# Kernel optimization log

Measured on AMD Instinct MI355X. Metric: run time of the kernel, lower is better.

Reference implementation:

```python
import jax, jax.numpy as jnp
import numpy as np

H, D_IN, D_Q, D_V = 8, 16, 32, 32
N = M = 4096


def setup_inputs() -> dict:
    key = jax.random.key(0)
    ks = jax.random.split(key, 12)
    s_in = 1.0 / np.sqrt(D_IN)
    s_fc = 1.0 / np.sqrt(H * D_V)
    return {
        "x": jax.random.normal(ks[0], (N, D_IN), jnp.float32),
        "y": jax.random.normal(ks[1], (M, D_IN), jnp.float32),
        # per-head stacked weights: [H, D_IN, D_Q/ D_V]
        "Wq": jax.random.uniform(ks[2], (H, D_IN, D_Q), jnp.float32, -s_in, s_in),
        "bq": jax.random.uniform(ks[3], (H, D_Q), jnp.float32, -s_in, s_in),
        "Wk": jax.random.uniform(ks[4], (H, D_IN, D_Q), jnp.float32, -s_in, s_in),
        "bk": jax.random.uniform(ks[5], (H, D_Q), jnp.float32, -s_in, s_in),
        "Wv": jax.random.uniform(ks[6], (H, D_IN, D_V), jnp.float32, -s_in, s_in),
        "bv": jax.random.uniform(ks[7], (H, D_V), jnp.float32, -s_in, s_in),
        "Wo": jax.random.uniform(ks[8], (H * D_V, D_IN), jnp.float32, -s_fc, s_fc),
        "bo": jax.random.uniform(ks[9], (D_IN,), jnp.float32, -s_fc, s_fc),
    }


def reference(x, y, Wq, bq, Wk, bk, Wv, bv, Wo, bo):
    # batched per-head projections (fuses the 8 tiny Linears of the torch loop)
    q = jnp.einsum("nd,hdq->hnq", x, Wq) + bq[:, None, :]   # [H, N, D_Q]
    k = jnp.einsum("md,hdq->hmq", y, Wk) + bk[:, None, :]   # [H, M, D_Q]
    v = jnp.einsum("md,hdv->hmv", y, Wv) + bv[:, None, :]   # [H, M, D_V]
    scores = jnp.einsum("hnq,hmq->hnm", q, k) / jnp.sqrt(jnp.float32(D_Q))
    attn = jax.nn.softmax(scores, axis=-1)                  # [H, N, M]
    heads = jnp.einsum("hnm,hmv->hnv", attn, v)             # [H, N, D_V]
    # torch.cat(head_outputs, dim=-1): head h occupies columns [h*D_V:(h+1)*D_V]
    concat = jnp.transpose(heads, (1, 0, 2)).reshape(x.shape[0], H * D_V)
    return concat @ Wo + bo                                  # [N, D_IN]
```

## Files before the change

kernel.cpp:

```cpp
#include <hip/hip_runtime.h>
#include <hip/hip_bf16.h>

typedef __attribute__((ext_vector_type(8))) short bf16x8;
typedef __attribute__((ext_vector_type(4))) float f32x4;
typedef unsigned short u16;
typedef unsigned int u32;

#define NH 8
#define NN 4096
#define MM 4096

__device__ __forceinline__ u16 f2bf(float f) {
  u32 b = __float_as_uint(f);
  b += 0x7FFFu + ((b >> 16) & 1u);
  return (u16)(b >> 16);
}

__device__ __forceinline__ u32 pack_rnu(float a, float b) {
  u32 ua = __float_as_uint(a) + 0x8000u;
  u32 ub = __float_as_uint(b) + 0x8000u;
#if __has_builtin(__builtin_amdgcn_perm)
  return __builtin_amdgcn_perm(ub, ua, 0x07060302u);
#else
  return (ua >> 16) | (ub & 0xFFFF0000u);
#endif
}

#if __has_builtin(__builtin_amdgcn_exp2f)
__device__ __forceinline__ float exp2_fast(float x) { return __builtin_amdgcn_exp2f(x); }
#else
__device__ __forceinline__ float exp2_fast(float x) { return __expf(x * 0.69314718055994531f); }
#endif

__global__ __launch_bounds__(256) void proj_kernel(
    const float* __restrict__ x, const float* __restrict__ y,
    const float* __restrict__ Wq, const float* __restrict__ bq,
    const float* __restrict__ Wk, const float* __restrict__ bk,
    const float* __restrict__ Wv, const float* __restrict__ bv,
    u16* __restrict__ qs, u16* __restrict__ ks, u16* __restrict__ vT)
{
  __shared__ u16 sv[256][33];
  const int bid = blockIdx.x;
  const int tid = threadIdx.x;
  if (bid < 256) {
    int idx = bid * 256 + tid;
    int t = idx >> 15;
    int h = (idx >> 12) & 7;
    int row = idx & 4095;
    const float* src = (t ? y : x) + row * 16;
    const float* W = (t ? Wk : Wq) + (h << 9);
    const float* b = (t ? bk : bq) + (h << 5);
    const float scale = t ? 1.0f : 0.25503635116465163f;
    float4 r4[4];
#pragma unroll
    for (int i = 0; i < 4; ++i) r4[i] = ((const float4*)src)[i];
    const float* r = (const float*)r4;
    u16* out = (t ? ks : qs) + (idx & 32767) * 32;
#pragma unroll
    for (int j = 0; j < 32; ++j) {
      float a = b[j];
#pragma unroll
      for (int i = 0; i < 16; ++i) a = fmaf(r[i], W[i * 32 + j], a);
      out[j] = f2bf(a * scale);
    }
  } else {
    int vb = bid - 256;
    int h = vb >> 4;
    int kb = (vb & 15) << 8;
    const float* src = y + (kb + tid) * 16;
    const float* W = Wv + (h << 9);
    const float* b = bv + (h << 5);
    float4 r4[4];
#pragma unroll
    for (int i = 0; i < 4; ++i) r4[i] = ((const float4*)src)[i];
    const float* r = (const float*)r4;
#pragma unroll
    for (int j = 0; j < 32; ++j) {
      float a = b[j];
#pragma unroll
      for (int i = 0; i < 16; ++i) a = fmaf(r[i], W[i * 32 + j], a);
      sv[tid][j] = f2bf(a);
    }
    __syncthreads();
    int dv = tid >> 3;
    int c = (tid & 7) << 5;
    u16* dst = vT + (((h << 5) + dv) << 12) + kb + c;
#pragma unroll
    for (int q = 0; q < 4; ++q) {
      uint4 w;
      w.x = (u32)sv[c + 4 * q + 0][dv]      | ((u32)sv[c + 4 * q + 1][dv] << 16);
      w.y = (u32)sv[c + 4 * q + 2][dv]      | ((u32)sv[c + 4 * q + 3][dv] << 16);
      w.z = (u32)sv[c + 16 + 4 * q + 0][dv] | ((u32)sv[c + 16 + 4 * q + 1][dv] << 16);
      w.w = (u32)sv[c + 16 + 4 * q + 2][dv] | ((u32)sv[c + 16 + 4 * q + 3][dv] << 16);
      *(uint4*)(dst + q * 8) = w;
    }
  }
}

#define KST 40
#define VST 72
#define VSZ (32 * VST)

__global__ __launch_bounds__(256) void flash_kernel(
    const u16* __restrict__ qs, const u16* __restrict__ ksrc,
    const u16* __restrict__ vT, float* __restrict__ accP,
    float* __restrict__ lsumP)
{
  __shared__ u16 sK[128 * KST];
  __shared__ u16 sVT[2 * VSZ];
  const int h = blockIdx.y;
  const int qt = blockIdx.x;
  const int z = blockIdx.z;
  const int nIter = (MM / 128) / gridDim.z;
  const int kb0 = z * (MM / gridDim.z);
  const int tid = threadIdx.x;
  const int wv = tid >> 6;
  const int lane = tid & 63;
  const int d = lane & 15;
  const int g = lane >> 4;
  const int qrowA = (qt << 7) + (wv << 5) + d;
  const int qrowB = qrowA + 16;

  union U4 { uint4 q; bf16x8 v; };
  U4 qfA, qfB;
  qfA.q = *(const uint4*)(qs + (((h << 12) + qrowA) << 5) + (g << 3));
  qfB.q = *(const uint4*)(qs + (((h << 12) + qrowB) << 5) + (g << 3));

  float lsA = 0.f, lsB = 0.f;
  f32x4 accA0 = {0.f, 0.f, 0.f, 0.f}, accA1 = {0.f, 0.f, 0.f, 0.f};
  f32x4 accB0 = {0.f, 0.f, 0.f, 0.f}, accB1 = {0.f, 0.f, 0.f, 0.f};
  const f32x4 zero = {0.f, 0.f, 0.f, 0.f};

  const u16* gK = ksrc + (h << 17) + (kb0 << 5) + ((tid >> 1) << 5) + ((tid & 1) << 4);
  const u16* gV = vT + (((h << 5) + (tid >> 3)) << 12) + kb0 + ((tid & 7) << 4);
  u16* wK = sK + (tid >> 1) * KST + ((tid & 1) << 4);
  u16* wV = sVT + ((tid & 7) >> 2) * VSZ + (tid >> 3) * VST + ((tid & 7) & 3) * 16;

  {
    uint4 a = *(const uint4*)gK, b = *(const uint4*)(gK + 8);
    uint4 c = *(const uint4*)gV, e = *(const uint4*)(gV + 8);
    *(uint4*)wK = a; *(uint4*)(wK + 8) = b;
    *(uint4*)wV = c; *(uint4*)(wV + 8) = e;
  }
  __syncthreads();

  auto compute = [&](const u16* kb, const u16* vb) {
    U4 kf0, kf1, kf2, kf3;
    kf0.q = *(const uint4*)(kb + (0 * 16 + d) * KST + (g << 3));
    kf1.q = *(const uint4*)(kb + (1 * 16 + d) * KST + (g << 3));
    kf2.q = *(const uint4*)(kb + (2 * 16 + d) * KST + (g << 3));
    kf3.q = *(const uint4*)(kb + (3 * 16 + d) * KST + (g << 3));
    U4 vf0, vf1, vf2, vf3;
    {
      const u16* vp = vb + d * VST;
      vf0.q = *(const uint4*)(vp + (g << 3));
      vf1.q = *(const uint4*)(vp + 32 + (g << 3));
      vp += 16 * VST;
      vf2.q = *(const uint4*)(vp + (g << 3));
      vf3.q = *(const uint4*)(vp + 32 + (g << 3));
    }
#define QTILE(QF, ACC0, ACC1, LS)                                              \
    {                                                                          \
      f32x4 s0, s1, s2, s3;                                                    \
      s0 = __builtin_amdgcn_mfma_f32_16x16x32_bf16(kf0.v, QF.v, zero, 0, 0, 0);\
      s1 = __builtin_amdgcn_mfma_f32_16x16x32_bf16(kf1.v, QF.v, zero, 0, 0, 0);\
      s2 = __builtin_amdgcn_mfma_f32_16x16x32_bf16(kf2.v, QF.v, zero, 0, 0, 0);\
      s3 = __builtin_amdgcn_mfma_f32_16x16x32_bf16(kf3.v, QF.v, zero, 0, 0, 0);\
      float e0 = exp2_fast(s0.x), e1 = exp2_fast(s0.y);                        \
      float e2 = exp2_fast(s0.z), e3 = exp2_fast(s0.w);                        \
      float e4 = exp2_fast(s1.x), e5 = exp2_fast(s1.y);                        \
      float e6 = exp2_fast(s1.z), e7 = exp2_fast(s1.w);                        \
      float e8 = exp2_fast(s2.x), e9 = exp2_fast(s2.y);                        \
      float e10 = exp2_fast(s2.z), e11 = exp2_fast(s2.w);                      \
      float e12 = exp2_fast(s3.x), e13 = exp2_fast(s3.y);                      \
      float e14 = exp2_fast(s3.z), e15 = exp2_fast(s3.w);                      \
      LS += (((e0 + e1) + (e2 + e3)) + ((e4 + e5) + (e6 + e7)))                \
          + (((e8 + e9) + (e10 + e11)) + ((e12 + e13) + (e14 + e15)));         \
      union { u32 w[4]; bf16x8 v; } pb0, pb1;                                  \
      pb0.w[0] = pack_rnu(e0, e1);   pb0.w[1] = pack_rnu(e2, e3);              \
      pb0.w[2] = pack_rnu(e4, e5);   pb0.w[3] = pack_rnu(e6, e7);              \
      pb1.w[0] = pack_rnu(e8, e9);   pb1.w[1] = pack_rnu(e10, e11);            \
      pb1.w[2] = pack_rnu(e12, e13); pb1.w[3] = pack_rnu(e14, e15);            \
      ACC0 = __builtin_amdgcn_mfma_f32_16x16x32_bf16(vf0.v, pb0.v, ACC0, 0, 0, 0); \
      ACC0 = __builtin_amdgcn_mfma_f32_16x16x32_bf16(vf1.v, pb1.v, ACC0, 0, 0, 0); \
      ACC1 = __builtin_amdgcn_mfma_f32_16x16x32_bf16(vf2.v, pb0.v, ACC1, 0, 0, 0); \
      ACC1 = __builtin_amdgcn_mfma_f32_16x16x32_bf16(vf3.v, pb1.v, ACC1, 0, 0, 0); \
    }
    QTILE(qfA, accA0, accA1, lsA)
    QTILE(qfB, accB0, accB1, lsB)
#undef QTILE
  };

#pragma unroll 1
  for (int it = 0; it < nIter; ++it) {
    uint4 a, b, c, e;
    if (it < nIter - 1) {
      gK += 4096; gV += 128;
      a = *(const uint4*)gK; b = *(const uint4*)(gK + 8);
      c = *(const uint4*)gV; e = *(const uint4*)(gV + 8);
    }
    compute(sK, sVT);
    compute(sK + 64 * KST, sVT + VSZ);
    __syncthreads();
    if (it < nIter - 1) {
      *(uint4*)wK = a; *(uint4*)(wK + 8) = b;
      *(uint4*)wV = c; *(uint4*)(wV + 8) = e;
      __syncthreads();
    }
  }

  lsA += __shfl_xor(lsA, 16);  lsA += __shfl_xor(lsA, 32);
  lsB += __shfl_xor(lsB, 16);  lsB += __shfl_xor(lsB, 32);
  if (g == 0) {
    lsumP[((z * NH + h) << 12) + qrowA] = lsA;
    lsumP[((z * NH + h) << 12) + qrowB] = lsB;
  }
  float* cpA = accP + z * (NN * 256) + (qrowA << 8) + (h << 5) + (g << 2);
  *(float4*)cpA        = make_float4(accA0.x, accA0.y, accA0.z, accA0.w);
  *(float4*)(cpA + 16) = make_float4(accA1.x, accA1.y, accA1.z, accA1.w);
  float* cpB = accP + z * (NN * 256) + (qrowB << 8) + (h << 5) + (g << 2);
  *(float4*)cpB        = make_float4(accB0.x, accB0.y, accB0.z, accB0.w);
  *(float4*)(cpB + 16) = make_float4(accB1.x, accB1.y, accB1.z, accB1.w);
}

__global__ __launch_bounds__(256) void out_fused_kernel(
    const float* __restrict__ accP, const float* __restrict__ lsumP,
    const float* __restrict__ Wo, const float* __restrict__ bo,
    float* __restrict__ out, int S)
{
  __shared__ float cn[4][256];
  __shared__ float sQ[4][4][16];
  const int tid = threadIdx.x;
  const int n0 = blockIdx.x << 2;

  {
    const int r = tid >> 6, u = tid & 63;
    const int n = n0 + r;
    float4 o = make_float4(0.f, 0.f, 0.f, 0.f);
    for (int s = 0; s < S; ++s) {
      const float4 v = *(const float4*)(accP + (size_t)s * (NN * 256) + (n << 8) + (u << 2));
      o.x += v.x; o.y += v.y; o.z += v.z; o.w += v.w;
    }
    const int hh = u >> 3;
    float l = 0.f;
    for (int s = 0; s < S; ++s) l += lsumP[((s * NH + hh) << 12) + n];
    const float inv = 1.0f / l;
    *(float4*)&cn[r][u << 2] = make_float4(o.x * inv, o.y * inv, o.z * inv, o.w * inv);
  }
  __syncthreads();

  {
    const int r = tid >> 6, ks = (tid >> 4) & 3, c = tid & 15;
    const float* cr = &cn[r][ks << 6];
    const float* wp = Wo + (ks << 6) * 16 + c;
    float a = 0.f;
#pragma unroll
    for (int jj = 0; jj < 64; ++jj) {
      const int j2 = (jj + (ks << 4)) & 63;
      a = fmaf(cr[j2], wp[j2 * 16], a);
    }
    sQ[r][ks][c] = a;
  }
  __syncthreads();

  if (tid < 64) {
    const int r = tid >> 4, c = tid & 15;
    float v = bo[c] + ((sQ[r][0][c] + sQ[r][1][c]) + (sQ[r][2][c] + sQ[r][3][c]));
    out[((n0 + r) << 4) + c] = v;
  }
}

extern "C" void kernel_launch(void* const* d_in, const int* in_sizes, int n_in,
                              void* d_out, int out_size, void* d_ws, size_t ws_size,
                              hipStream_t stream) {
  const float* x  = (const float*)d_in[0];
  const float* y  = (const float*)d_in[1];
  const float* Wq = (const float*)d_in[2];
  const float* bq = (const float*)d_in[3];
  const float* Wk = (const float*)d_in[4];
  const float* bk = (const float*)d_in[5];
  const float* Wv = (const float*)d_in[6];
  const float* bv = (const float*)d_in[7];
  const float* Wo = (const float*)d_in[8];
  const float* bo = (const float*)d_in[9];
  float* out = (float*)d_out;

  u16* qs = (u16*)d_ws;
  u16* ks = qs + (NH * NN * 32);
  u16* vT = ks + (NH * MM * 32);
  float* accP = (float*)(vT + (NH * MM * 32));
  int S = 1;
  if (ws_size >= (size_t)(6 + 32 + 2) * 1024 * 1024) S = 8;
  else if (ws_size >= (size_t)(6 + 16 + 1) * 1024 * 1024) S = 4;
  float* lsumP = accP + (size_t)S * (NN * 256);

  hipLaunchKernelGGL(proj_kernel, dim3(384), dim3(256), 0, stream,
                     x, y, Wq, bq, Wk, bk, Wv, bv, qs, ks, vT);
  hipLaunchKernelGGL(flash_kernel, dim3(32, NH, S), dim3(256), 0, stream,
                     qs, ks, vT, accP, lsumP);
  hipLaunchKernelGGL(out_fused_kernel, dim3(1024), dim3(256), 0, stream,
                     accP, lsumP, Wo, bo, out, S);
}
```

Measured before the change: 66.79 us.

## Load flash K/V fragments straight from global and split output stage

The flash kernel stops staging K and V tiles through shared memory. Each wave now loads its MFMA fragments directly from global memory and prefetches the next 64-key step into registers, which removes the LDS writes and both per-iteration __syncthreads. The grid is flattened with the head index varying fastest, and the key split is fixed at 4. The fused output kernel is replaced by an in-place combine kernel plus a separate output GEMM that keeps Wo in LDS. The cost is that the four waves of a block each read the same K/V from global or L2, one more kernel launch is added, and S=4 no longer adapts to the workspace size.

```diff
diff --git a/kernel.cpp b/kernel.cpp
--- a/kernel.cpp
+++ b/kernel.cpp
@@ -97,22 +97,16 @@
   }
 }
 
-#define KST 40
-#define VST 72
-#define VSZ (32 * VST)
-
 __global__ __launch_bounds__(256) void flash_kernel(
     const u16* __restrict__ qs, const u16* __restrict__ ksrc,
     const u16* __restrict__ vT, float* __restrict__ accP,
     float* __restrict__ lsumP)
 {
-  __shared__ u16 sK[128 * KST];
-  __shared__ u16 sVT[2 * VSZ];
-  const int h = blockIdx.y;
-  const int qt = blockIdx.x;
-  const int z = blockIdx.z;
-  const int nIter = (MM / 128) / gridDim.z;
-  const int kb0 = z * (MM / gridDim.z);
+  const int bid = blockIdx.x;
+  const int h = bid & 7;
+  const int qt = (bid >> 3) & 31;
+  const int z = bid >> 8;
+  const int kb0 = z << 10;
   const int tid = threadIdx.x;
   const int wv = tid >> 6;
   const int lane = tid & 63;
@@ -131,33 +125,32 @@
   f32x4 accB0 = {0.f, 0.f, 0.f, 0.f}, accB1 = {0.f, 0.f, 0.f, 0.f};
   const f32x4 zero = {0.f, 0.f, 0.f, 0.f};
 
-  const u16* gK = ksrc + (h << 17) + (kb0 << 5) + ((tid >> 1) << 5) + ((tid & 1) << 4);
-  const u16* gV = vT + (((h << 5) + (tid >> 3)) << 12) + kb0 + ((tid & 7) << 4);
-  u16* wK = sK + (tid >> 1) * KST + ((tid & 1) << 4);
-  u16* wV = sVT + ((tid & 7) >> 2) * VSZ + (tid >> 3) * VST + ((tid & 7) & 3) * 16;
-
-  {
-    uint4 a = *(const uint4*)gK, b = *(const uint4*)(gK + 8);
-    uint4 c = *(const uint4*)gV, e = *(const uint4*)(gV + 8);
-    *(uint4*)wK = a; *(uint4*)(wK + 8) = b;
-    *(uint4*)wV = c; *(uint4*)(wV + 8) = e;
-  }
-  __syncthreads();
-
-  auto compute = [&](const u16* kb, const u16* vb) {
-    U4 kf0, kf1, kf2, kf3;
-    kf0.q = *(const uint4*)(kb + (0 * 16 + d) * KST + (g << 3));
-    kf1.q = *(const uint4*)(kb + (1 * 16 + d) * KST + (g << 3));
-    kf2.q = *(const uint4*)(kb + (2 * 16 + d) * KST + (g << 3));
-    kf3.q = *(const uint4*)(kb + (3 * 16 + d) * KST + (g << 3));
-    U4 vf0, vf1, vf2, vf3;
-    {
-      const u16* vp = vb + d * VST;
-      vf0.q = *(const uint4*)(vp + (g << 3));
-      vf1.q = *(const uint4*)(vp + 32 + (g << 3));
-      vp += 16 * VST;
-      vf2.q = *(const uint4*)(vp + (g << 3));
-      vf3.q = *(const uint4*)(vp + 32 + (g << 3));
+  const u16* kp = ksrc + (h << 17) + ((kb0 + d) << 5) + (g << 3);
+  const u16* vp = vT + (((h << 5) + d) << 12) + kb0 + (g << 3);
+
+  U4 kf0, kf1, kf2, kf3, vf0, vf1, vf2, vf3;
+  kf0.q = *(const uint4*)(kp);
+  kf1.q = *(const uint4*)(kp + 512);
+  kf2.q = *(const uint4*)(kp + 1024);
+  kf3.q = *(const uint4*)(kp + 1536);
+  vf0.q = *(const uint4*)(vp);
+  vf1.q = *(const uint4*)(vp + 32);
+  vf2.q = *(const uint4*)(vp + (16 << 12));
+  vf3.q = *(const uint4*)(vp + (16 << 12) + 32);
+
+#pragma unroll 1
+  for (int it = 0; it < 16; ++it) {
+    U4 nk0, nk1, nk2, nk3, nv0, nv1, nv2, nv3;
+    if (it < 15) {
+      kp += 2048; vp += 64;
+      nk0.q = *(const uint4*)(kp);
+      nk1.q = *(const uint4*)(kp + 512);
+      nk2.q = *(const uint4*)(kp + 1024);
+      nk3.q = *(const uint4*)(kp + 1536);
+      nv0.q = *(const uint4*)(vp);
+      nv1.q = *(const uint4*)(vp + 32);
+      nv2.q = *(const uint4*)(vp + (16 << 12));
+      nv3.q = *(const uint4*)(vp + (16 << 12) + 32);
     }
 #define QTILE(QF, ACC0, ACC1, LS)                                              \
     {                                                                          \
@@ -189,23 +182,9 @@
     QTILE(qfA, accA0, accA1, lsA)
     QTILE(qfB, accB0, accB1, lsB)
 #undef QTILE
-  };
-
-#pragma unroll 1
-  for (int it = 0; it < nIter; ++it) {
-    uint4 a, b, c, e;
-    if (it < nIter - 1) {
-      gK += 4096; gV += 128;
-      a = *(const uint4*)gK; b = *(const uint4*)(gK + 8);
-      c = *(const uint4*)gV; e = *(const uint4*)(gV + 8);
-    }
-    compute(sK, sVT);
-    compute(sK + 64 * KST, sVT + VSZ);
-    __syncthreads();
-    if (it < nIter - 1) {
-      *(uint4*)wK = a; *(uint4*)(wK + 8) = b;
-      *(uint4*)wV = c; *(uint4*)(wV + 8) = e;
-      __syncthreads();
+    if (it < 15) {
+      kf0 = nk0; kf1 = nk1; kf2 = nk2; kf3 = nk3;
+      vf0 = nv0; vf1 = nv1; vf2 = nv2; vf3 = nv3;
     }
   }
 
@@ -223,51 +202,43 @@
   *(float4*)(cpB + 16) = make_float4(accB1.x, accB1.y, accB1.z, accB1.w);
 }
 
-__global__ __launch_bounds__(256) void out_fused_kernel(
+__global__ __launch_bounds__(256) void combine_kernel(
     const float* __restrict__ accP, const float* __restrict__ lsumP,
-    const float* __restrict__ Wo, const float* __restrict__ bo,
-    float* __restrict__ out, int S)
-{
-  __shared__ float cn[4][256];
-  __shared__ float sQ[4][4][16];
-  const int tid = threadIdx.x;
-  const int n0 = blockIdx.x << 2;
-
-  {
-    const int r = tid >> 6, u = tid & 63;
-    const int n = n0 + r;
-    float4 o = make_float4(0.f, 0.f, 0.f, 0.f);
-    for (int s = 0; s < S; ++s) {
-      const float4 v = *(const float4*)(accP + (size_t)s * (NN * 256) + (n << 8) + (u << 2));
-      o.x += v.x; o.y += v.y; o.z += v.z; o.w += v.w;
-    }
-    const int hh = u >> 3;
-    float l = 0.f;
-    for (int s = 0; s < S; ++s) l += lsumP[((s * NH + hh) << 12) + n];
-    const float inv = 1.0f / l;
-    *(float4*)&cn[r][u << 2] = make_float4(o.x * inv, o.y * inv, o.z * inv, o.w * inv);
-  }
+    float* __restrict__ concat, int S)
+{
+  int idx = blockIdx.x * 256 + threadIdx.x;
+  int n = idx >> 8;
+  int h = (idx & 255) >> 5;
+  float o = 0.f, l = 0.f;
+  for (int s = 0; s < S; ++s) {
+    o += accP[s * (NN * 256) + idx];
+    l += lsumP[((s * NH + h) << 12) + n];
+  }
+  concat[idx] = o / l;
+}
+
+__global__ __launch_bounds__(256) void out_gemm_kernel(
+    const float* __restrict__ concat, const float* __restrict__ Wo,
+    const float* __restrict__ bo, float* __restrict__ out)
+{
+  __shared__ float sWo[4096];
+  int tid = threadIdx.x;
+  for (int i = tid; i < 4096; i += 256) sWo[i] = Wo[i];
   __syncthreads();
-
-  {
-    const int r = tid >> 6, ks = (tid >> 4) & 3, c = tid & 15;
-    const float* cr = &cn[r][ks << 6];
-    const float* wp = Wo + (ks << 6) * 16 + c;
-    float a = 0.f;
-#pragma unroll
-    for (int jj = 0; jj < 64; ++jj) {
-      const int j2 = (jj + (ks << 4)) & 63;
-      a = fmaf(cr[j2], wp[j2 * 16], a);
-    }
-    sQ[r][ks][c] = a;
-  }
-  __syncthreads();
-
-  if (tid < 64) {
-    const int r = tid >> 4, c = tid & 15;
-    float v = bo[c] + ((sQ[r][0][c] + sQ[r][1][c]) + (sQ[r][2][c] + sQ[r][3][c]));
-    out[((n0 + r) << 4) + c] = v;
-  }
+  int idx = blockIdx.x * 256 + tid;
+  int n = idx >> 4;
+  int c = idx & 15;
+  const float4* crow = (const float4*)(concat + (n << 8));
+  float a = bo[c];
+#pragma unroll 4
+  for (int i4 = 0; i4 < 64; ++i4) {
+    float4 cv = crow[i4];
+    a = fmaf(cv.x, sWo[(i4 * 4 + 0) * 16 + c], a);
+    a = fmaf(cv.y, sWo[(i4 * 4 + 1) * 16 + c], a);
+    a = fmaf(cv.z, sWo[(i4 * 4 + 2) * 16 + c], a);
+    a = fmaf(cv.w, sWo[(i4 * 4 + 3) * 16 + c], a);
+  }
+  out[idx] = a;
 }
 
 extern "C" void kernel_launch(void* const* d_in, const int* in_sizes, int n_in,
@@ -288,16 +259,16 @@
   u16* qs = (u16*)d_ws;
   u16* ks = qs + (NH * NN * 32);
   u16* vT = ks + (NH * MM * 32);
-  float* accP = (float*)(vT + (NH * MM * 32));
-  int S = 1;
-  if (ws_size >= (size_t)(6 + 32 + 2) * 1024 * 1024) S = 8;
-  else if (ws_size >= (size_t)(6 + 16 + 1) * 1024 * 1024) S = 4;
+  float* concat = (float*)(vT + (NH * MM * 32));
+  float* accP = concat;
+  const int S = 4;
   float* lsumP = accP + (size_t)S * (NN * 256);
 
   hipLaunchKernelGGL(proj_kernel, dim3(384), dim3(256), 0, stream,
                      x, y, Wq, bq, Wk, bk, Wv, bv, qs, ks, vT);
-  hipLaunchKernelGGL(flash_kernel, dim3(32, NH, S), dim3(256), 0, stream,
+  hipLaunchKernelGGL(flash_kernel, dim3(32 * NH * S), dim3(256), 0, stream,
                      qs, ks, vT, accP, lsumP);
-  hipLaunchKernelGGL(out_fused_kernel, dim3(1024), dim3(256), 0, stream,
-                     accP, lsumP, Wo, bo, out, S);
-}
+  hipLaunchKernelGGL(combine_kernel, dim3(4096), dim3(256), 0, stream,
+                     accP, lsumP, concat, S);
+  hipLaunchKernelGGL(out_gemm_kernel, dim3(256), dim3(256), 0, stream, concat, Wo, bo, out);
+}
```

New measurement: 81.53 us. 1.22x slower.
